# Kernel tuning notes

Measured on AMD Instinct MI355X. Metric: run time of the kernel, lower is better.

Reference implementation:

```python
import jax, jax.numpy as jnp
import numpy as np

N, D_IN, D_H, D_ATT, C_CLUST, N_CLS = 10000, 1024, 512, 256, 10, 4


def setup_inputs() -> dict:
    key = jax.random.key(0)
    ks = jax.random.split(key, 20)
    s = 0.02
    return {
        "x": jax.random.normal(ks[0], (N, D_IN), dtype=jnp.float32),
        "cluster_id": jax.random.randint(ks[1], (N,), 0, C_CLUST, dtype=jnp.int64),
        # per-cluster phi: Linear(1024->512) + ReLU + Linear(512->512) + ReLU
        "W1": s * jax.random.normal(ks[2], (C_CLUST, D_IN, D_H), dtype=jnp.float32),
        "b1": jnp.zeros((C_CLUST, D_H), dtype=jnp.float32),
        "W2": s * jax.random.normal(ks[3], (C_CLUST, D_H, D_H), dtype=jnp.float32),
        "b2": jnp.zeros((C_CLUST, D_H), dtype=jnp.float32),
        # attention_net fc: Linear(512->512)+ReLU
        "Wfc": s * jax.random.normal(ks[4], (D_H, D_H), dtype=jnp.float32),
        "bfc": jnp.zeros((D_H,), dtype=jnp.float32),
        # Attn_Net_Gated
        "Wa": s * jax.random.normal(ks[5], (D_H, D_ATT), dtype=jnp.float32),
        "ba": jnp.zeros((D_ATT,), dtype=jnp.float32),
        "Wb": s * jax.random.normal(ks[6], (D_H, D_ATT), dtype=jnp.float32),
        "bb": jnp.zeros((D_ATT,), dtype=jnp.float32),
        "Wc": s * jax.random.normal(ks[7], (D_ATT, 1), dtype=jnp.float32),
        "bc": jnp.zeros((1,), dtype=jnp.float32),
        # rho: Linear(512->256)+ReLU
        "Wr": s * jax.random.normal(ks[8], (D_H, D_ATT), dtype=jnp.float32),
        "br": jnp.zeros((D_ATT,), dtype=jnp.float32),
        # classifier: Linear(256->4)
        "Wcls": s * jax.random.normal(ks[9], (D_ATT, N_CLS), dtype=jnp.float32),
        "bcls": jnp.zeros((N_CLS,), dtype=jnp.float32),
    }


def reference(x, cluster_id, W1, b1, W2, b2, Wfc, bfc, Wa, ba, Wb, bb, Wc, bc, Wr, br, Wcls, bcls):
    C = W1.shape[0]
    # dense dispatch: apply every cluster's phi, then masked-mean per cluster
    # (ReLU is per-point elementwise, so masked mean == mean over members)
    h1 = jax.nn.relu(jnp.einsum('nd,cdh->cnh', x, W1) + b1[:, None, :])   # [C,N,512]
    h2 = jax.nn.relu(jnp.einsum('cnh,chk->cnk', h1, W2) + b2[:, None, :]) # [C,N,512]
    mask = (cluster_id[None, :] == jnp.arange(C)[:, None]).astype(h2.dtype)  # [C,N]
    counts = jnp.maximum(mask.sum(axis=1), 1.0)                           # [C]
    pooled = jnp.einsum('cnk,cn->ck', h2, mask) / counts[:, None]         # [C,512]
    # attention_net: fc + gated attention
    h = jax.nn.relu(pooled @ Wfc + bfc)                                   # [C,512]
    gate = jnp.tanh(h @ Wa + ba) * jax.nn.sigmoid(h @ Wb + bb)            # [C,256]
    A = (gate @ Wc + bc)                                                  # [C,1]
    A = jax.nn.softmax(A.T, axis=1)                                       # [1,C]
    h_path = A @ h                                                        # [1,512]
    hr = jax.nn.relu(h_path @ Wr + br)                                    # [1,256]
    logits = (hr[0] @ Wcls + bcls)[None, :]                               # [1,4]
    Y_prob = jax.nn.softmax(logits, axis=1)
    Y_hat = jnp.argmax(logits, axis=1)[:, None]
    return logits, Y_prob, Y_hat
```

## Files before the change

kernel.cpp:

```cpp
#include <hip/hip_runtime.h>
#include <math.h>

#define DIN 1024
#define DH 512
#define DATT 256
#define CNUM 10
#define NCLS 4

typedef __attribute__((ext_vector_type(8))) short bf16x8;
typedef __attribute__((ext_vector_type(4))) float f32x4;
typedef unsigned short ushort_t;
typedef unsigned int uint_t;

__device__ inline ushort_t f2bf(float f) {
    uint_t u = __float_as_uint(f);
    u += 0x7FFF + ((u >> 16) & 1);
    return (ushort_t)(u >> 16);
}

__device__ inline void gl_lds16(const void* g, void* l) {
    __builtin_amdgcn_global_load_lds(
        (const __attribute__((address_space(1))) unsigned int*)g,
        (__attribute__((address_space(3))) unsigned int*)l, 16, 0, 0);
}


__global__ __launch_bounds__(1024) void k_bucket(
    const int* __restrict__ cid, int n, const float* __restrict__ bc,
    int* __restrict__ counts_g, int* __restrict__ offsets_g, int* __restrict__ tile_off_g,
    int* __restrict__ bucket, float* __restrict__ pooled, float* __restrict__ a_logit)
{
    __shared__ int h[CNUM], off[CNUM + 1], cur[CNUM], toff[CNUM + 1];
    int t = threadIdx.x;
    int lane = t & 63;
    if (t < CNUM) { h[t] = 0; cur[t] = 0; }
    __syncthreads();

    for (int i = t; i < n; i += 1024) {
        int c = cid[i];
        #pragma unroll
        for (int cc = 0; cc < CNUM; cc++) {
            unsigned long long mask = __ballot(c == cc);
            if (mask == 0ull) continue;
            int leader = __ffsll(mask) - 1;
            if (lane == leader) atomicAdd(&h[cc], __popcll(mask));
        }
    }
    __syncthreads();
    if (t == 0) {
        int a = 0, tt = 0;
        for (int c = 0; c < CNUM; c++) {
            off[c] = a; toff[c] = tt;
            a += h[c]; tt += (h[c] + 127) >> 7;
        }
        off[CNUM] = a; toff[CNUM] = tt;
    }
    __syncthreads();
    if (t < CNUM) counts_g[t] = h[t];
    if (t <= CNUM) { offsets_g[t] = off[t]; tile_off_g[t] = toff[t]; }
    if (t < CNUM) a_logit[t] = bc[0];

    for (int i = t; i < n; i += 1024) {
        int c = cid[i];
        #pragma unroll
        for (int cc = 0; cc < CNUM; cc++) {
            unsigned long long mask = __ballot(c == cc);
            if (mask == 0ull) continue;
            int leader = __ffsll(mask) - 1;
            int basep = 0;
            if (lane == leader) basep = atomicAdd(&cur[cc], __popcll(mask));
            basep = __shfl(basep, leader, 64);
            if (c == cc) {
                int rank = __popcll(mask & ((1ull << lane) - 1ull));
                bucket[off[cc] + basep + rank] = i;
            }
        }
    }
    for (int i = t; i < CNUM * DH; i += 1024) pooled[i] = 0.f;
}


__global__ __launch_bounds__(256) void k_castx(
    const float* __restrict__ x, const int* __restrict__ bucket,
    ushort_t* __restrict__ xb, int n)
{
    int row = blockIdx.x * 2 + (threadIdx.x >> 7);
    if (row >= n) return;
    int col = (threadIdx.x & 127) * 8;
    const float* src = x + (size_t)bucket[row] * DIN + col;
    float4 v0 = *(const float4*)(src);
    float4 v1 = *(const float4*)(src + 4);
    ushort4 o0 = make_ushort4(f2bf(v0.x), f2bf(v0.y), f2bf(v0.z), f2bf(v0.w));
    ushort4 o1 = make_ushort4(f2bf(v1.x), f2bf(v1.y), f2bf(v1.z), f2bf(v1.w));
    ushort_t* dst = xb + (size_t)row * DIN + col;
    *(ushort4*)dst = o0;
    *(ushort4*)(dst + 4) = o1;
}

__global__ __launch_bounds__(256) void k_castw(
    const float* __restrict__ W1, const float* __restrict__ W2,
    ushort_t* __restrict__ W1t, ushort_t* __restrict__ W2t)
{
    __shared__ float tile[64][65];
    int z = blockIdx.z;
    const float* src; ushort_t* dst; int K;
    if (z < CNUM) { K = DIN; src = W1 + (size_t)z * K * DH; dst = W1t + (size_t)z * DH * K; }
    else          { K = DH;  src = W2 + (size_t)(z - CNUM) * K * DH; dst = W2t + (size_t)(z - CNUM) * DH * K; }
    int k0 = blockIdx.x * 64;
    if (k0 >= K) return;
    int n0 = blockIdx.y * 64;
    int t = threadIdx.x;
    int rr = t >> 4;
    int cc = (t & 15) * 4;
    #pragma unroll
    for (int i = 0; i < 4; i++) {
        int row = rr + 16 * i;
        float4 v = *(const float4*)(src + (size_t)(k0 + row) * DH + n0 + cc);
        tile[row][cc + 0] = v.x; tile[row][cc + 1] = v.y;
        tile[row][cc + 2] = v.z; tile[row][cc + 3] = v.w;
    }
    __syncthreads();
    #pragma unroll
    for (int i = 0; i < 4; i++) {
        int nrow = rr + 16 * i;
        ushort4 o = make_ushort4(f2bf(tile[cc + 0][nrow]), f2bf(tile[cc + 1][nrow]),
                                 f2bf(tile[cc + 2][nrow]), f2bf(tile[cc + 3][nrow]));
        *(ushort4*)(dst + (size_t)(n0 + nrow) * K + k0 + cc) = o;
    }
}


__device__ inline void gemm_tile(
    const ushort_t* __restrict__ A, const ushort_t* __restrict__ Wt,
    int Kd, int base, int cnt, int m0, int tile_n, int c,
    f32x4 acc[4][4], ushort_t As[128][32], ushort_t Bs[128][32])
{
    int t = threadIdx.x;
    int lane = t & 63;
    int w = t >> 6, wr = w >> 1, wc = w & 1;
    int m = lane & 15, quad = lane >> 4;

    int r0 = t >> 2;
    int kc = (t & 3) * 8;

    int ra0 = m0 + r0;      if (ra0 > cnt - 1) ra0 = cnt - 1;
    int ra1 = m0 + 64 + r0; if (ra1 > cnt - 1) ra1 = cnt - 1;
    const ushort_t* aSrc0 = A + (size_t)(base + ra0) * Kd + kc;
    const ushort_t* aSrc1 = A + (size_t)(base + ra1) * Kd + kc;
    const ushort_t* bSrc0 = Wt + ((size_t)c * DH + tile_n + r0) * Kd + kc;
    const ushort_t* bSrc1 = Wt + ((size_t)c * DH + tile_n + 64 + r0) * Kd + kc;

    ushort_t* aDst0 = &As[r0][kc];
    ushort_t* aDst1 = &As[64 + r0][kc];
    ushort_t* bDst0 = &Bs[r0][kc];
    ushort_t* bDst1 = &Bs[64 + r0][kc];

    const ushort_t* aF = &As[64 * wr + m][quad * 8];
    const ushort_t* bF = &Bs[64 * wc + m][quad * 8];

    for (int k0 = 0; k0 < Kd; k0 += 32) {
        __syncthreads();
        gl_lds16(aSrc0 + k0, aDst0);
        gl_lds16(aSrc1 + k0, aDst1);
        gl_lds16(bSrc0 + k0, bDst0);
        gl_lds16(bSrc1 + k0, bDst1);
        __syncthreads();
        bf16x8 a[4], b[4];
        #pragma unroll
        for (int mf = 0; mf < 4; mf++) a[mf] = *(const bf16x8*)(aF + mf * 16 * 32);
        #pragma unroll
        for (int nf = 0; nf < 4; nf++) b[nf] = *(const bf16x8*)(bF + nf * 16 * 32);
        #pragma unroll
        for (int mf = 0; mf < 4; mf++)
            #pragma unroll
            for (int nf = 0; nf < 4; nf++)
                acc[mf][nf] = __builtin_amdgcn_mfma_f32_16x16x32_bf16(a[mf], b[nf], acc[mf][nf], 0, 0, 0);
    }
}

__global__ __launch_bounds__(256, 1) void k_mfma1(
    const ushort_t* __restrict__ xb, const ushort_t* __restrict__ W1t,
    const float* __restrict__ b1,
    const int* __restrict__ offsets, const int* __restrict__ counts,
    const int* __restrict__ tile_off,
    ushort_t* __restrict__ H1)
{
    __shared__ ushort_t As[128][32];
    __shared__ ushort_t Bs[128][32];
    int tx = blockIdx.x;
    if (tx >= tile_off[CNUM]) return;
    int c = 0;
    while (tx >= tile_off[c + 1]) c++;
    int m0 = (tx - tile_off[c]) * 128;
    int base = offsets[c], cnt = counts[c];
    int tile_n = blockIdx.y * 128;

    f32x4 acc[4][4] = {};
    gemm_tile(xb, W1t, DIN, base, cnt, m0, tile_n, c, acc, As, Bs);

    int t = threadIdx.x, lane = t & 63;
    int w = t >> 6, wr = w >> 1, wc = w & 1;
    int m = lane & 15, quad = lane >> 4;
    int col0 = tile_n + 64 * wc;
    #pragma unroll
    for (int nf = 0; nf < 4; nf++) {
        int col = col0 + 16 * nf + m;
        float bv = b1[c * DH + col];
        #pragma unroll
        for (int mf = 0; mf < 4; mf++) {
            int rowb = m0 + 64 * wr + 16 * mf + quad * 4;
            #pragma unroll
            for (int r = 0; r < 4; r++) {
                int row = rowb + r;
                if (row < cnt)
                    H1[(size_t)(base + row) * DH + col] = f2bf(fmaxf(acc[mf][nf][r] + bv, 0.f));
            }
        }
    }
}

__global__ __launch_bounds__(256, 1) void k_mfma2(
    const ushort_t* __restrict__ H1, const ushort_t* __restrict__ W2t,
    const float* __restrict__ b2,
    const int* __restrict__ offsets, const int* __restrict__ counts,
    const int* __restrict__ tile_off,
    float* __restrict__ pooled)
{
    __shared__ ushort_t As[128][32];
    __shared__ ushort_t Bs[128][32];
    int tx = blockIdx.x;
    if (tx >= tile_off[CNUM]) return;
    int c = 0;
    while (tx >= tile_off[c + 1]) c++;
    int m0 = (tx - tile_off[c]) * 128;
    int base = offsets[c], cnt = counts[c];
    int tile_n = blockIdx.y * 128;

    f32x4 acc[4][4] = {};
    gemm_tile(H1, W2t, DH, base, cnt, m0, tile_n, c, acc, As, Bs);

    int t = threadIdx.x, lane = t & 63;
    int w = t >> 6, wr = w >> 1, wc = w & 1;
    int m = lane & 15, quad = lane >> 4;
    int col0 = tile_n + 64 * wc;
    #pragma unroll
    for (int nf = 0; nf < 4; nf++) {
        int col = col0 + 16 * nf + m;
        float bv = b2[c * DH + col];
        float s = 0.f;
        #pragma unroll
        for (int mf = 0; mf < 4; mf++) {
            int rowb = m0 + 64 * wr + 16 * mf + quad * 4;
            #pragma unroll
            for (int r = 0; r < 4; r++) {
                int row = rowb + r;
                if (row < cnt) s += fmaxf(acc[mf][nf][r] + bv, 0.f);
            }
        }
        s += __shfl_xor(s, 16);
        s += __shfl_xor(s, 32);
        if (quad == 0) atomicAdd(&pooled[c * DH + col], s);
    }
}


#define MT 64
#define NT 128
#define KT 32

__global__ __launch_bounds__(256) void k_gemm1(
    const float* __restrict__ x, const float* __restrict__ W1, const float* __restrict__ b1,
    const int* __restrict__ bucket, const int* __restrict__ offsets, const int* __restrict__ counts,
    float* __restrict__ H1)
{
    int c = blockIdx.z;
    int cnt = counts[c];
    int m0 = blockIdx.x * MT;
    if (m0 >= cnt) return;
    int rows = min(MT, cnt - m0);
    int n0 = blockIdx.y * NT;
    int base = offsets[c];

    __shared__ float As[KT][MT + 4];
    __shared__ float Bs[KT][NT];

    int t = threadIdx.x;
    int tr = t >> 4;
    int tc = t & 15;
    int lr = t >> 2;
    int lk = (t & 3) * 8;
    const float* xrow = nullptr;
    if (lr < rows) xrow = x + (size_t)bucket[base + m0 + lr] * DIN;

    float acc[4][8];
    #pragma unroll
    for (int i = 0; i < 4; i++)
        #pragma unroll
        for (int j = 0; j < 8; j++) acc[i][j] = 0.f;

    const float* Wp = W1 + (size_t)c * DIN * DH + n0;

    for (int k0 = 0; k0 < DIN; k0 += KT) {
        __syncthreads();
        if (xrow) {
            float4 v0 = *(const float4*)(xrow + k0 + lk);
            float4 v1 = *(const float4*)(xrow + k0 + lk + 4);
            As[lk + 0][lr] = v0.x; As[lk + 1][lr] = v0.y;
            As[lk + 2][lr] = v0.z; As[lk + 3][lr] = v0.w;
            As[lk + 4][lr] = v1.x; As[lk + 5][lr] = v1.y;
            As[lk + 6][lr] = v1.z; As[lk + 7][lr] = v1.w;
        } else {
            #pragma unroll
            for (int i = 0; i < 8; i++) As[lk + i][lr] = 0.f;
        }
        #pragma unroll
        for (int i = 0; i < 4; i++) {
            int idx = i * 256 + t;
            int kk = idx >> 5;
            int cv = idx & 31;
            *(float4*)&Bs[kk][cv * 4] = *(const float4*)(Wp + (size_t)(k0 + kk) * DH + cv * 4);
        }
        __syncthreads();
        #pragma unroll
        for (int k = 0; k < KT; k++) {
            float4 av  = *(const float4*)&As[k][4 * tr];
            float4 bv0 = *(const float4*)&Bs[k][4 * tc];
            float4 bv1 = *(const float4*)&Bs[k][64 + 4 * tc];
            float a[4] = {av.x, av.y, av.z, av.w};
            float b[8] = {bv0.x, bv0.y, bv0.z, bv0.w, bv1.x, bv1.y, bv1.z, bv1.w};
            #pragma unroll
            for (int i = 0; i < 4; i++)
                #pragma unroll
                for (int j = 0; j < 8; j++)
                    acc[i][j] = fmaf(a[i], b[j], acc[i][j]);
        }
    }

    #pragma unroll
    for (int i = 0; i < 4; i++) {
        int r = 4 * tr + i;
        if (r < rows) {
            size_t grow = (size_t)(base + m0 + r) * DH;
            #pragma unroll
            for (int j = 0; j < 8; j++) {
                int cidx = (j < 4) ? (4 * tc + j) : (64 + 4 * tc + (j - 4));
                int col = n0 + cidx;
                float v = acc[i][j] + b1[c * DH + col];
                H1[grow + col] = fmaxf(v, 0.f);
            }
        }
    }
}

__global__ __launch_bounds__(256) void k_gemm2(
    const float* __restrict__ H1, const float* __restrict__ W2, const float* __restrict__ b2,
    const int* __restrict__ offsets, const int* __restrict__ counts,
    float* __restrict__ pooled)
{
    int c = blockIdx.z;
    int cnt = counts[c];
    int m0 = blockIdx.x * MT;
    if (m0 >= cnt) return;
    int rows = min(MT, cnt - m0);
    int n0 = blockIdx.y * NT;
    int base = offsets[c];

    __shared__ float As[KT][MT + 4];
    __shared__ float Bs[KT][NT];
    __shared__ float red[16][NT];

    int t = threadIdx.x;
    int tr = t >> 4;
    int tc = t & 15;
    int lr = t >> 2;
    int lk = (t & 3) * 8;
    const float* arow = (lr < rows) ? (H1 + (size_t)(base + m0 + lr) * DH) : nullptr;

    float acc[4][8];
    #pragma unroll
    for (int i = 0; i < 4; i++)
        #pragma unroll
        for (int j = 0; j < 8; j++) acc[i][j] = 0.f;

    const float* Wp = W2 + (size_t)c * DH * DH + n0;

    for (int k0 = 0; k0 < DH; k0 += KT) {
        __syncthreads();
        if (arow) {
            float4 v0 = *(const float4*)(arow + k0 + lk);
            float4 v1 = *(const float4*)(arow + k0 + lk + 4);
            As[lk + 0][lr] = v0.x; As[lk + 1][lr] = v0.y;
            As[lk + 2][lr] = v0.z; As[lk + 3][lr] = v0.w;
            As[lk + 4][lr] = v1.x; As[lk + 5][lr] = v1.y;
            As[lk + 6][lr] = v1.z; As[lk + 7][lr] = v1.w;
        } else {
            #pragma unroll
            for (int i = 0; i < 8; i++) As[lk + i][lr] = 0.f;
        }
        #pragma unroll
        for (int i = 0; i < 4; i++) {
            int idx = i * 256 + t;
            int kk = idx >> 5;
            int cv = idx & 31;
            *(float4*)&Bs[kk][cv * 4] = *(const float4*)(Wp + (size_t)(k0 + kk) * DH + cv * 4);
        }
        __syncthreads();
        #pragma unroll
        for (int k = 0; k < KT; k++) {
            float4 av  = *(const float4*)&As[k][4 * tr];
            float4 bv0 = *(const float4*)&Bs[k][4 * tc];
            float4 bv1 = *(const float4*)&Bs[k][64 + 4 * tc];
            float a[4] = {av.x, av.y, av.z, av.w};
            float b[8] = {bv0.x, bv0.y, bv0.z, bv0.w, bv1.x, bv1.y, bv1.z, bv1.w};
            #pragma unroll
            for (int i = 0; i < 4; i++)
                #pragma unroll
                for (int j = 0; j < 8; j++)
                    acc[i][j] = fmaf(a[i], b[j], acc[i][j]);
        }
    }

    __syncthreads();
    #pragma unroll
    for (int j = 0; j < 8; j++) {
        int cidx = (j < 4) ? (4 * tc + j) : (64 + 4 * tc + (j - 4));
        float bias = b2[c * DH + n0 + cidx];
        float s = 0.f;
        #pragma unroll
        for (int i = 0; i < 4; i++) {
            if (4 * tr + i < rows) s += fmaxf(acc[i][j] + bias, 0.f);
        }
        red[tr][cidx] = s;
    }
    __syncthreads();
    if (t < NT) {
        float s = 0.f;
        #pragma unroll
        for (int r = 0; r < 16; r++) s += red[r][t];
        atomicAdd(&pooled[c * DH + n0 + t], s);
    }
}


__global__ __launch_bounds__(256) void k_fc2(
    const float* __restrict__ pooled, const int* __restrict__ counts,
    const float* __restrict__ Wfc, const float* __restrict__ bfc,
    float* __restrict__ hfc)
{
    int c = blockIdx.x;
    int c0 = blockIdx.y * 64;
    __shared__ float ps[DH];
    __shared__ float red[4][64];
    int t = threadIdx.x;
    float cnt = fmaxf((float)counts[c], 1.f);
    ps[t] = pooled[c * DH + t] / cnt;
    ps[t + 256] = pooled[c * DH + t + 256] / cnt;
    __syncthreads();
    int col = c0 + (t & 63);
    int ks = t >> 6;
    float acc = 0.f;
    #pragma unroll 8
    for (int k = ks * 128; k < ks * 128 + 128; k++)
        acc = fmaf(ps[k], Wfc[(size_t)k * DH + col], acc);
    red[ks][t & 63] = acc;
    __syncthreads();
    if (t < 64) {
        float v = red[0][t] + red[1][t] + red[2][t] + red[3][t] + bfc[c0 + t];
        hfc[c * DH + c0 + t] = fmaxf(v, 0.f);
    }
}

__global__ __launch_bounds__(256) void k_gate2(
    const float* __restrict__ hfc,
    const float* __restrict__ Wa, const float* __restrict__ ba,
    const float* __restrict__ Wb, const float* __restrict__ bb,
    const float* __restrict__ Wc,
    float* __restrict__ a_logit)
{
    int c = blockIdx.x;
    int d0 = blockIdx.y * 64;
    __shared__ float hf[DH];
    __shared__ float ra[4][64], rb[4][64];
    int t = threadIdx.x;
    hf[t] = hfc[c * DH + t];
    hf[t + 256] = hfc[c * DH + t + 256];
    __syncthreads();
    int d = d0 + (t & 63);
    int ks = t >> 6;
    float ga = 0.f, gb = 0.f;
    #pragma unroll 8
    for (int k = ks * 128; k < ks * 128 + 128; k++) {
        float h = hf[k];
        ga = fmaf(h, Wa[(size_t)k * DATT + d], ga);
        gb = fmaf(h, Wb[(size_t)k * DATT + d], gb);
    }
    ra[ks][t & 63] = ga;
    rb[ks][t & 63] = gb;
    __syncthreads();
    if (t < 64) {
        float sa = ra[0][t] + ra[1][t] + ra[2][t] + ra[3][t] + ba[d0 + t];
        float sb = rb[0][t] + rb[1][t] + rb[2][t] + rb[3][t] + bb[d0 + t];
        float g = tanhf(sa) * (1.f / (1.f + expf(-sb)));
        float p = g * Wc[d0 + t];
        #pragma unroll
        for (int off = 32; off >= 1; off >>= 1) p += __shfl_down(p, off, 64);
        if (t == 0) atomicAdd(&a_logit[c], p);
    }
}

__global__ __launch_bounds__(1024) void k_final(
    const float* __restrict__ hfc, const float* __restrict__ a_logit,
    const float* __restrict__ Wr, const float* __restrict__ br,
    const float* __restrict__ Wcls, const float* __restrict__ bcls,
    float* __restrict__ out)
{
    int t = threadIdx.x;
    __shared__ float hp[DH];
    __shared__ float r1[4][DATT];
    __shared__ float hr[DATT];
    __shared__ float wred[4][NCLS];

    float al[CNUM];
    float m = -1e30f;
    #pragma unroll
    for (int c = 0; c < CNUM; c++) { al[c] = a_logit[c]; m = fmaxf(m, al[c]); }
    float s = 0.f;
    #pragma unroll
    for (int c = 0; c < CNUM; c++) { al[c] = expf(al[c] - m); s += al[c]; }
    float inv = 1.f / s;

    if (t < DH) {
        float v = 0.f;
        #pragma unroll
        for (int c = 0; c < CNUM; c++) v = fmaf(al[c] * inv, hfc[c * DH + t], v);
        hp[t] = v;
    }
    __syncthreads();

    int d = t & 255;
    int ks = t >> 8;
    float acc = 0.f;
    #pragma unroll 8
    for (int k = ks * 128; k < ks * 128 + 128; k++)
        acc = fmaf(hp[k], Wr[(size_t)k * DATT + d], acc);
    r1[ks][d] = acc;
    __syncthreads();
    if (t < DATT)
        hr[t] = fmaxf(r1[0][t] + r1[1][t] + r1[2][t] + r1[3][t] + br[t], 0.f);
    __syncthreads();

    if (t < 256) {
        float h = hr[t];
        #pragma unroll
        for (int cls = 0; cls < NCLS; cls++) {
            float p = h * Wcls[(size_t)t * NCLS + cls];
            #pragma unroll
            for (int off = 32; off >= 1; off >>= 1) p += __shfl_down(p, off, 64);
            if ((t & 63) == 0) wred[t >> 6][cls] = p;
        }
    }
    __syncthreads();
    if (t == 0) {
        float lg[NCLS];
        #pragma unroll
        for (int cls = 0; cls < NCLS; cls++)
            lg[cls] = bcls[cls] + wred[0][cls] + wred[1][cls] + wred[2][cls] + wred[3][cls];
        float mm = lg[0];
        #pragma unroll
        for (int i = 1; i < NCLS; i++) mm = fmaxf(mm, lg[i]);
        float ss = 0.f, pr[NCLS];
        #pragma unroll
        for (int i = 0; i < NCLS; i++) { pr[i] = expf(lg[i] - mm); ss += pr[i]; }
        int am = 0; float best = lg[0];
        #pragma unroll
        for (int i = 1; i < NCLS; i++) if (lg[i] > best) { best = lg[i]; am = i; }
        #pragma unroll
        for (int i = 0; i < NCLS; i++) out[i] = lg[i];
        #pragma unroll
        for (int i = 0; i < NCLS; i++) out[4 + i] = pr[i] / ss;
        out[8] = (float)am;
    }
}


extern "C" void kernel_launch(void* const* d_in, const int* in_sizes, int n_in,
                              void* d_out, int out_size, void* d_ws, size_t ws_size,
                              hipStream_t stream) {
    (void)n_in; (void)out_size;
    const float* x    = (const float*)d_in[0];
    const int*   cid  = (const int*)d_in[1];
    const float* W1   = (const float*)d_in[2];
    const float* b1   = (const float*)d_in[3];
    const float* W2   = (const float*)d_in[4];
    const float* b2   = (const float*)d_in[5];
    const float* Wfc  = (const float*)d_in[6];
    const float* bfc  = (const float*)d_in[7];
    const float* Wa   = (const float*)d_in[8];
    const float* ba   = (const float*)d_in[9];
    const float* Wb   = (const float*)d_in[10];
    const float* bb   = (const float*)d_in[11];
    const float* Wc   = (const float*)d_in[12];
    const float* bc   = (const float*)d_in[13];
    const float* Wr   = (const float*)d_in[14];
    const float* br   = (const float*)d_in[15];
    const float* Wcls = (const float*)d_in[16];
    const float* bcls = (const float*)d_in[17];
    float* out = (float*)d_out;
    float* ws  = (float*)d_ws;

    int n = in_sizes[1];

    float* pooled   = ws + 0;
    int*   counts   = (int*)(ws + 5120);
    int*   offsets  = (int*)(ws + 5136);
    int*   tile_off = (int*)(ws + 5152);
    float* a_logit  = ws + 5168;
    float* hfc      = ws + 5184;
    int*   bucket   = (int*)(ws + 10304);

    size_t big0 = (((size_t)(10304 + n) * 4) + 255) & ~(size_t)255;
    size_t w1t_bytes = (size_t)CNUM * DH * DIN * 2;
    size_t w2t_bytes = (size_t)CNUM * DH * DH * 2;
    size_t h1_bytes  = (size_t)n * DH * 2;
    size_t xb_bytes  = (size_t)n * DIN * 2;
    size_t need = big0 + w1t_bytes + w2t_bytes + h1_bytes + xb_bytes;

    k_bucket<<<1, 1024, 0, stream>>>(cid, n, bc, counts, offsets, tile_off, bucket, pooled, a_logit);

    if (ws_size >= need) {
        ushort_t* W1t = (ushort_t*)((char*)d_ws + big0);
        ushort_t* W2t = (ushort_t*)((char*)d_ws + big0 + w1t_bytes);
        ushort_t* H1  = (ushort_t*)((char*)d_ws + big0 + w1t_bytes + w2t_bytes);
        ushort_t* xb  = (ushort_t*)((char*)d_ws + big0 + w1t_bytes + w2t_bytes + h1_bytes);

        k_castx<<<(n + 1) / 2, 256, 0, stream>>>(x, bucket, xb, n);
        k_castw<<<dim3(DIN / 64, DH / 64, 2 * CNUM), 256, 0, stream>>>(W1, W2, W1t, W2t);

        int maxt = n / 128 + CNUM;
        k_mfma1<<<dim3(maxt, DH / 128), 256, 0, stream>>>(xb, W1t, b1, offsets, counts, tile_off, H1);
        k_mfma2<<<dim3(maxt, DH / 128), 256, 0, stream>>>(H1, W2t, b2, offsets, counts, tile_off, pooled);
    } else {
        float* H1f = ws + ((10304 + n + 31) & ~31);
        dim3 gg((n + MT - 1) / MT, DH / NT, CNUM);
        k_gemm1<<<gg, 256, 0, stream>>>(x, W1, b1, bucket, offsets, counts, H1f);
        k_gemm2<<<gg, 256, 0, stream>>>(H1f, W2, b2, offsets, counts, pooled);
    }

    k_fc2<<<dim3(CNUM, 8), 256, 0, stream>>>(pooled, counts, Wfc, bfc, hfc);
    k_gate2<<<dim3(CNUM, 4), 256, 0, stream>>>(hfc, Wa, ba, Wb, bb, Wc, a_logit);
    k_final<<<1, 1024, 0, stream>>>(hfc, a_logit, Wr, br, Wcls, bcls, out);
}
```

Before: 259.7 us.

## Fuse x cast, both phi GEMMs and pooling into one kernel

```diff
diff --git a/kernel.cpp b/kernel.cpp
--- a/kernel.cpp
+++ b/kernel.cpp
@@ -6,6 +6,7 @@
 #define DATT 256
 #define CNUM 10
 #define NCLS 4
+#define ROWS 32
 
 typedef __attribute__((ext_vector_type(8))) short bf16x8;
 typedef __attribute__((ext_vector_type(4))) float f32x4;
@@ -51,7 +52,7 @@
         int a = 0, tt = 0;
         for (int c = 0; c < CNUM; c++) {
             off[c] = a; toff[c] = tt;
-            a += h[c]; tt += (h[c] + 127) >> 7;
+            a += h[c]; tt += (h[c] + ROWS - 1) / ROWS;
         }
         off[CNUM] = a; toff[CNUM] = tt;
     }
@@ -80,23 +81,6 @@
 }
 
 
-__global__ __launch_bounds__(256) void k_castx(
-    const float* __restrict__ x, const int* __restrict__ bucket,
-    ushort_t* __restrict__ xb, int n)
-{
-    int row = blockIdx.x * 2 + (threadIdx.x >> 7);
-    if (row >= n) return;
-    int col = (threadIdx.x & 127) * 8;
-    const float* src = x + (size_t)bucket[row] * DIN + col;
-    float4 v0 = *(const float4*)(src);
-    float4 v1 = *(const float4*)(src + 4);
-    ushort4 o0 = make_ushort4(f2bf(v0.x), f2bf(v0.y), f2bf(v0.z), f2bf(v0.w));
-    ushort4 o1 = make_ushort4(f2bf(v1.x), f2bf(v1.y), f2bf(v1.z), f2bf(v1.w));
-    ushort_t* dst = xb + (size_t)row * DIN + col;
-    *(ushort4*)dst = o0;
-    *(ushort4*)(dst + 4) = o1;
-}
-
 __global__ __launch_bounds__(256) void k_castw(
     const float* __restrict__ W1, const float* __restrict__ W2,
     ushort_t* __restrict__ W1t, ushort_t* __restrict__ W2t)
@@ -130,136 +114,136 @@
 }
 
 
-__device__ inline void gemm_tile(
-    const ushort_t* __restrict__ A, const ushort_t* __restrict__ Wt,
-    int Kd, int base, int cnt, int m0, int tile_n, int c,
-    f32x4 acc[4][4], ushort_t As[128][32], ushort_t Bs[128][32])
-{
-    int t = threadIdx.x;
-    int lane = t & 63;
-    int w = t >> 6, wr = w >> 1, wc = w & 1;
-    int m = lane & 15, quad = lane >> 4;
-
-    int r0 = t >> 2;
-    int kc = (t & 3) * 8;
-
-    int ra0 = m0 + r0;      if (ra0 > cnt - 1) ra0 = cnt - 1;
-    int ra1 = m0 + 64 + r0; if (ra1 > cnt - 1) ra1 = cnt - 1;
-    const ushort_t* aSrc0 = A + (size_t)(base + ra0) * Kd + kc;
-    const ushort_t* aSrc1 = A + (size_t)(base + ra1) * Kd + kc;
-    const ushort_t* bSrc0 = Wt + ((size_t)c * DH + tile_n + r0) * Kd + kc;
-    const ushort_t* bSrc1 = Wt + ((size_t)c * DH + tile_n + 64 + r0) * Kd + kc;
-
-    ushort_t* aDst0 = &As[r0][kc];
-    ushort_t* aDst1 = &As[64 + r0][kc];
-    ushort_t* bDst0 = &Bs[r0][kc];
-    ushort_t* bDst1 = &Bs[64 + r0][kc];
-
-    const ushort_t* aF = &As[64 * wr + m][quad * 8];
-    const ushort_t* bF = &Bs[64 * wc + m][quad * 8];
-
-    for (int k0 = 0; k0 < Kd; k0 += 32) {
-        __syncthreads();
-        gl_lds16(aSrc0 + k0, aDst0);
-        gl_lds16(aSrc1 + k0, aDst1);
-        gl_lds16(bSrc0 + k0, bDst0);
-        gl_lds16(bSrc1 + k0, bDst1);
-        __syncthreads();
-        bf16x8 a[4], b[4];
-        #pragma unroll
-        for (int mf = 0; mf < 4; mf++) a[mf] = *(const bf16x8*)(aF + mf * 16 * 32);
-        #pragma unroll
-        for (int nf = 0; nf < 4; nf++) b[nf] = *(const bf16x8*)(bF + nf * 16 * 32);
-        #pragma unroll
-        for (int mf = 0; mf < 4; mf++)
-            #pragma unroll
-            for (int nf = 0; nf < 4; nf++)
-                acc[mf][nf] = __builtin_amdgcn_mfma_f32_16x16x32_bf16(a[mf], b[nf], acc[mf][nf], 0, 0, 0);
-    }
-}
-
-__global__ __launch_bounds__(256, 1) void k_mfma1(
-    const ushort_t* __restrict__ xb, const ushort_t* __restrict__ W1t,
-    const float* __restrict__ b1,
+__global__ __launch_bounds__(256, 1) void k_phi(
+    const float* __restrict__ x, const int* __restrict__ bucket,
+    const ushort_t* __restrict__ W1t, const ushort_t* __restrict__ W2t,
+    const float* __restrict__ b1, const float* __restrict__ b2,
     const int* __restrict__ offsets, const int* __restrict__ counts,
     const int* __restrict__ tile_off,
-    ushort_t* __restrict__ H1)
-{
-    __shared__ ushort_t As[128][32];
-    __shared__ ushort_t Bs[128][32];
+    float* __restrict__ pooled)
+{
+    __shared__ ushort_t As[ROWS][32];
+    __shared__ ushort_t Bs[256][32];
+    __shared__ ushort_t H1s[16][ROWS][32];
+
     int tx = blockIdx.x;
     if (tx >= tile_off[CNUM]) return;
     int c = 0;
     while (tx >= tile_off[c + 1]) c++;
-    int m0 = (tx - tile_off[c]) * 128;
+    int m0 = (tx - tile_off[c]) * ROWS;
     int base = offsets[c], cnt = counts[c];
-    int tile_n = blockIdx.y * 128;
-
-    f32x4 acc[4][4] = {};
-    gemm_tile(xb, W1t, DIN, base, cnt, m0, tile_n, c, acc, As, Bs);
 
     int t = threadIdx.x, lane = t & 63;
-    int w = t >> 6, wr = w >> 1, wc = w & 1;
+    int w = t >> 6;
     int m = lane & 15, quad = lane >> 4;
-    int col0 = tile_n + 64 * wc;
-    #pragma unroll
-    for (int nf = 0; nf < 4; nf++) {
-        int col = col0 + 16 * nf + m;
-        float bv = b1[c * DH + col];
-        #pragma unroll
-        for (int mf = 0; mf < 4; mf++) {
-            int rowb = m0 + 64 * wr + 16 * mf + quad * 4;
-            #pragma unroll
-            for (int r = 0; r < 4; r++) {
-                int row = rowb + r;
-                if (row < cnt)
-                    H1[(size_t)(base + row) * DH + col] = f2bf(fmaxf(acc[mf][nf][r] + bv, 0.f));
+
+    int ar = t >> 3;
+    int akc = (t & 7) * 4;
+    int arow = m0 + ar; if (arow > cnt - 1) arow = cnt - 1;
+    const float* aPtr = x + (size_t)bucket[base + arow] * DIN + akc;
+
+    char* bsDst = (char*)&Bs[0][0] + 16 * t;
+    int bRow = t >> 2;
+    int bKc = (t & 3) * 8;
+
+    const ushort_t* aF0 = &As[m][quad * 8];
+    const ushort_t* aF1 = &As[16 + m][quad * 8];
+    const ushort_t* bF  = &Bs[64 * w + m][quad * 8];
+
+    f32x4 acc[2][4];
+
+    #pragma unroll
+    for (int p = 0; p < 2; p++) {
+        #pragma unroll
+        for (int mf = 0; mf < 2; mf++)
+            #pragma unroll
+            for (int nf = 0; nf < 4; nf++) acc[mf][nf] = (f32x4)(0.f);
+
+        const ushort_t* wp = W1t + ((size_t)c * DH + p * 256 + bRow) * DIN + bKc;
+
+        for (int k0 = 0; k0 < DIN; k0 += 32) {
+            __syncthreads();
+            float4 av = *(const float4*)(aPtr + k0);
+            *(ushort4*)&As[ar][akc] =
+                make_ushort4(f2bf(av.x), f2bf(av.y), f2bf(av.z), f2bf(av.w));
+            #pragma unroll
+            for (int i = 0; i < 4; i++)
+                gl_lds16(wp + k0 + (size_t)(64 * i) * DIN, bsDst + 4096 * i);
+            __syncthreads();
+
+            bf16x8 a0 = *(const bf16x8*)aF0;
+            bf16x8 a1 = *(const bf16x8*)aF1;
+            bf16x8 b[4];
+            #pragma unroll
+            for (int nf = 0; nf < 4; nf++) b[nf] = *(const bf16x8*)(bF + nf * 512);
+            #pragma unroll
+            for (int nf = 0; nf < 4; nf++) {
+                acc[0][nf] = __builtin_amdgcn_mfma_f32_16x16x32_bf16(a0, b[nf], acc[0][nf], 0, 0, 0);
+                acc[1][nf] = __builtin_amdgcn_mfma_f32_16x16x32_bf16(a1, b[nf], acc[1][nf], 0, 0, 0);
             }
         }
-    }
-}
-
-__global__ __launch_bounds__(256, 1) void k_mfma2(
-    const ushort_t* __restrict__ H1, const ushort_t* __restrict__ W2t,
-    const float* __restrict__ b2,
-    const int* __restrict__ offsets, const int* __restrict__ counts,
-    const int* __restrict__ tile_off,
-    float* __restrict__ pooled)
-{
-    __shared__ ushort_t As[128][32];
-    __shared__ ushort_t Bs[128][32];
-    int tx = blockIdx.x;
-    if (tx >= tile_off[CNUM]) return;
-    int c = 0;
-    while (tx >= tile_off[c + 1]) c++;
-    int m0 = (tx - tile_off[c]) * 128;
-    int base = offsets[c], cnt = counts[c];
-    int tile_n = blockIdx.y * 128;
-
-    f32x4 acc[4][4] = {};
-    gemm_tile(H1, W2t, DH, base, cnt, m0, tile_n, c, acc, As, Bs);
-
-    int t = threadIdx.x, lane = t & 63;
-    int w = t >> 6, wr = w >> 1, wc = w & 1;
-    int m = lane & 15, quad = lane >> 4;
-    int col0 = tile_n + 64 * wc;
-    #pragma unroll
-    for (int nf = 0; nf < 4; nf++) {
-        int col = col0 + 16 * nf + m;
-        float bv = b2[c * DH + col];
-        float s = 0.f;
-        #pragma unroll
-        for (int mf = 0; mf < 4; mf++) {
-            int rowb = m0 + 64 * wr + 16 * mf + quad * 4;
-            #pragma unroll
-            for (int r = 0; r < 4; r++) {
-                int row = rowb + r;
-                if (row < cnt) s += fmaxf(acc[mf][nf][r] + bv, 0.f);
+
+        #pragma unroll
+        for (int nf = 0; nf < 4; nf++) {
+            int colL = 64 * w + 16 * nf + m;
+            int col = p * 256 + colL;
+            float bv = b1[c * DH + col];
+            int chunk = p * 8 + (colL >> 5);
+            int ck = colL & 31;
+            #pragma unroll
+            for (int mf = 0; mf < 2; mf++)
+                #pragma unroll
+                for (int r = 0; r < 4; r++)
+                    H1s[chunk][16 * mf + quad * 4 + r][ck] =
+                        f2bf(fmaxf(acc[mf][nf][r] + bv, 0.f));
+        }
+    }
+
+    #pragma unroll
+    for (int p = 0; p < 2; p++) {
+        #pragma unroll
+        for (int mf = 0; mf < 2; mf++)
+            #pragma unroll
+            for (int nf = 0; nf < 4; nf++) acc[mf][nf] = (f32x4)(0.f);
+
+        const ushort_t* wp = W2t + ((size_t)c * DH + p * 256 + bRow) * DH + bKc;
+
+        for (int k0 = 0; k0 < DH; k0 += 32) {
+            __syncthreads();
+            #pragma unroll
+            for (int i = 0; i < 4; i++)
+                gl_lds16(wp + k0 + (size_t)(64 * i) * DH, bsDst + 4096 * i);
+            __syncthreads();
+
+            const ushort_t* h = &H1s[k0 >> 5][0][0];
+            bf16x8 a0 = *(const bf16x8*)(h + m * 32 + quad * 8);
+            bf16x8 a1 = *(const bf16x8*)(h + (16 + m) * 32 + quad * 8);
+            bf16x8 b[4];
+            #pragma unroll
+            for (int nf = 0; nf < 4; nf++) b[nf] = *(const bf16x8*)(bF + nf * 512);
+            #pragma unroll
+            for (int nf = 0; nf < 4; nf++) {
+                acc[0][nf] = __builtin_amdgcn_mfma_f32_16x16x32_bf16(a0, b[nf], acc[0][nf], 0, 0, 0);
+                acc[1][nf] = __builtin_amdgcn_mfma_f32_16x16x32_bf16(a1, b[nf], acc[1][nf], 0, 0, 0);
             }
         }
-        s += __shfl_xor(s, 16);
-        s += __shfl_xor(s, 32);
-        if (quad == 0) atomicAdd(&pooled[c * DH + col], s);
+
+        #pragma unroll
+        for (int nf = 0; nf < 4; nf++) {
+            int col = p * 256 + 64 * w + 16 * nf + m;
+            float bv = b2[c * DH + col];
+            float s = 0.f;
+            #pragma unroll
+            for (int mf = 0; mf < 2; mf++)
+                #pragma unroll
+                for (int r = 0; r < 4; r++) {
+                    int row = m0 + 16 * mf + quad * 4 + r;
+                    if (row < cnt) s += fmaxf(acc[mf][nf][r] + bv, 0.f);
+                }
+            s += __shfl_xor(s, 16);
+            s += __shfl_xor(s, 32);
+            if (quad == 0) atomicAdd(&pooled[c * DH + col], s);
+        }
     }
 }
 
@@ -621,24 +605,19 @@
     size_t big0 = (((size_t)(10304 + n) * 4) + 255) & ~(size_t)255;
     size_t w1t_bytes = (size_t)CNUM * DH * DIN * 2;
     size_t w2t_bytes = (size_t)CNUM * DH * DH * 2;
-    size_t h1_bytes  = (size_t)n * DH * 2;
-    size_t xb_bytes  = (size_t)n * DIN * 2;
-    size_t need = big0 + w1t_bytes + w2t_bytes + h1_bytes + xb_bytes;
+    size_t need = big0 + w1t_bytes + w2t_bytes;
 
     k_bucket<<<1, 1024, 0, stream>>>(cid, n, bc, counts, offsets, tile_off, bucket, pooled, a_logit);
 
     if (ws_size >= need) {
         ushort_t* W1t = (ushort_t*)((char*)d_ws + big0);
         ushort_t* W2t = (ushort_t*)((char*)d_ws + big0 + w1t_bytes);
-        ushort_t* H1  = (ushort_t*)((char*)d_ws + big0 + w1t_bytes + w2t_bytes);
-        ushort_t* xb  = (ushort_t*)((char*)d_ws + big0 + w1t_bytes + w2t_bytes + h1_bytes);
-
-        k_castx<<<(n + 1) / 2, 256, 0, stream>>>(x, bucket, xb, n);
+
         k_castw<<<dim3(DIN / 64, DH / 64, 2 * CNUM), 256, 0, stream>>>(W1, W2, W1t, W2t);
 
-        int maxt = n / 128 + CNUM;
-        k_mfma1<<<dim3(maxt, DH / 128), 256, 0, stream>>>(xb, W1t, b1, offsets, counts, tile_off, H1);
-        k_mfma2<<<dim3(maxt, DH / 128), 256, 0, stream>>>(H1, W2t, b2, offsets, counts, tile_off, pooled);
+        int maxt = (n + ROWS - 1) / ROWS + CNUM;
+        k_phi<<<maxt, 256, 0, stream>>>(x, bucket, W1t, W2t, b1, b2,
+                                        offsets, counts, tile_off, pooled);
     } else {
         float* H1f = ws + ((10304 + n + 31) & ~31);
         dim3 gg((n + MT - 1) / MT, DH / NT, CNUM);
```

After: 277.0 us. +6.7%, slower.

## Fuse bucketing and bf16 casts into one prep kernel, gather rows in GEMM1

Applied to the files above, without the earlier changes.

```diff
diff --git a/kernel.cpp b/kernel.cpp
--- a/kernel.cpp
+++ b/kernel.cpp
@@ -25,91 +25,97 @@
 }
 
 
-__global__ __launch_bounds__(1024) void k_bucket(
-    const int* __restrict__ cid, int n, const float* __restrict__ bc,
+__global__ __launch_bounds__(256) void k_prep(
+    const float* __restrict__ x, const int* __restrict__ cid, int n,
+    const float* __restrict__ bc,
+    const float* __restrict__ W1, const float* __restrict__ W2,
+    ushort_t* __restrict__ xb, ushort_t* __restrict__ W1t, ushort_t* __restrict__ W2t,
+    int do_cast,
     int* __restrict__ counts_g, int* __restrict__ offsets_g, int* __restrict__ tile_off_g,
     int* __restrict__ bucket, float* __restrict__ pooled, float* __restrict__ a_logit)
 {
-    __shared__ int h[CNUM], off[CNUM + 1], cur[CNUM], toff[CNUM + 1];
-    int t = threadIdx.x;
-    int lane = t & 63;
-    if (t < CNUM) { h[t] = 0; cur[t] = 0; }
-    __syncthreads();
-
-    for (int i = t; i < n; i += 1024) {
-        int c = cid[i];
-        #pragma unroll
-        for (int cc = 0; cc < CNUM; cc++) {
-            unsigned long long mask = __ballot(c == cc);
-            if (mask == 0ull) continue;
-            int leader = __ffsll(mask) - 1;
-            if (lane == leader) atomicAdd(&h[cc], __popcll(mask));
-        }
-    }
-    __syncthreads();
-    if (t == 0) {
-        int a = 0, tt = 0;
-        for (int c = 0; c < CNUM; c++) {
-            off[c] = a; toff[c] = tt;
-            a += h[c]; tt += (h[c] + 127) >> 7;
-        }
-        off[CNUM] = a; toff[CNUM] = tt;
-    }
-    __syncthreads();
-    if (t < CNUM) counts_g[t] = h[t];
-    if (t <= CNUM) { offsets_g[t] = off[t]; tile_off_g[t] = toff[t]; }
-    if (t < CNUM) a_logit[t] = bc[0];
-
-    for (int i = t; i < n; i += 1024) {
-        int c = cid[i];
-        #pragma unroll
-        for (int cc = 0; cc < CNUM; cc++) {
-            unsigned long long mask = __ballot(c == cc);
-            if (mask == 0ull) continue;
-            int leader = __ffsll(mask) - 1;
-            int basep = 0;
-            if (lane == leader) basep = atomicAdd(&cur[cc], __popcll(mask));
-            basep = __shfl(basep, leader, 64);
-            if (c == cc) {
-                int rank = __popcll(mask & ((1ull << lane) - 1ull));
-                bucket[off[cc] + basep + rank] = i;
+    int bid = blockIdx.x;
+    int t = threadIdx.x;
+
+    if (bid == 0) {
+        __shared__ int h[CNUM], off[CNUM + 1], cur[CNUM], toff[CNUM + 1];
+        int lane = t & 63;
+        if (t < CNUM) { h[t] = 0; cur[t] = 0; }
+        __syncthreads();
+
+        for (int i = t; i < n; i += 256) {
+            int c = cid[i];
+            #pragma unroll
+            for (int cc = 0; cc < CNUM; cc++) {
+                unsigned long long mask = __ballot(c == cc);
+                if (mask == 0ull) continue;
+                int leader = __ffsll(mask) - 1;
+                if (lane == leader) atomicAdd(&h[cc], __popcll(mask));
             }
         }
-    }
-    for (int i = t; i < CNUM * DH; i += 1024) pooled[i] = 0.f;
-}
-
-
-__global__ __launch_bounds__(256) void k_castx(
-    const float* __restrict__ x, const int* __restrict__ bucket,
-    ushort_t* __restrict__ xb, int n)
-{
-    int row = blockIdx.x * 2 + (threadIdx.x >> 7);
-    if (row >= n) return;
-    int col = (threadIdx.x & 127) * 8;
-    const float* src = x + (size_t)bucket[row] * DIN + col;
-    float4 v0 = *(const float4*)(src);
-    float4 v1 = *(const float4*)(src + 4);
-    ushort4 o0 = make_ushort4(f2bf(v0.x), f2bf(v0.y), f2bf(v0.z), f2bf(v0.w));
-    ushort4 o1 = make_ushort4(f2bf(v1.x), f2bf(v1.y), f2bf(v1.z), f2bf(v1.w));
-    ushort_t* dst = xb + (size_t)row * DIN + col;
-    *(ushort4*)dst = o0;
-    *(ushort4*)(dst + 4) = o1;
-}
-
-__global__ __launch_bounds__(256) void k_castw(
-    const float* __restrict__ W1, const float* __restrict__ W2,
-    ushort_t* __restrict__ W1t, ushort_t* __restrict__ W2t)
-{
+        __syncthreads();
+        if (t == 0) {
+            int a = 0, tt = 0;
+            for (int c = 0; c < CNUM; c++) {
+                off[c] = a; toff[c] = tt;
+                a += h[c]; tt += (h[c] + 127) >> 7;
+            }
+            off[CNUM] = a; toff[CNUM] = tt;
+        }
+        __syncthreads();
+        if (t < CNUM) counts_g[t] = h[t];
+        if (t <= CNUM) { offsets_g[t] = off[t]; tile_off_g[t] = toff[t]; }
+        if (t < CNUM) a_logit[t] = bc[0];
+
+        for (int i = t; i < n; i += 256) {
+            int c = cid[i];
+            #pragma unroll
+            for (int cc = 0; cc < CNUM; cc++) {
+                unsigned long long mask = __ballot(c == cc);
+                if (mask == 0ull) continue;
+                int leader = __ffsll(mask) - 1;
+                int basep = 0;
+                if (lane == leader) basep = atomicAdd(&cur[cc], __popcll(mask));
+                basep = __shfl(basep, leader, 64);
+                if (c == cc) {
+                    int rank = __popcll(mask & ((1ull << lane) - 1ull));
+                    bucket[off[cc] + basep + rank] = i;
+                }
+            }
+        }
+        for (int i = t; i < CNUM * DH; i += 256) pooled[i] = 0.f;
+        return;
+    }
+
+    if (!do_cast) return;
+
+    int nxb = (n + 1) / 2;
+    int idx = bid - 1;
+    if (idx < nxb) {
+        int row = idx * 2 + (t >> 7);
+        if (row >= n) return;
+        int col = (t & 127) * 8;
+        const float* src = x + (size_t)row * DIN + col;
+        float4 v0 = *(const float4*)(src);
+        float4 v1 = *(const float4*)(src + 4);
+        ushort_t* dst = xb + (size_t)row * DIN + col;
+        *(ushort4*)dst = make_ushort4(f2bf(v0.x), f2bf(v0.y), f2bf(v0.z), f2bf(v0.w));
+        *(ushort4*)(dst + 4) = make_ushort4(f2bf(v1.x), f2bf(v1.y), f2bf(v1.z), f2bf(v1.w));
+        return;
+    }
+
     __shared__ float tile[64][65];
-    int z = blockIdx.z;
+    int widx = idx - nxb;
+    int z = widx >> 7;
+    if (z >= 2 * CNUM) return;
+    int kx = (widx & 127) >> 3;
+    int ny = widx & 7;
     const float* src; ushort_t* dst; int K;
     if (z < CNUM) { K = DIN; src = W1 + (size_t)z * K * DH; dst = W1t + (size_t)z * DH * K; }
     else          { K = DH;  src = W2 + (size_t)(z - CNUM) * K * DH; dst = W2t + (size_t)(z - CNUM) * DH * K; }
-    int k0 = blockIdx.x * 64;
+    int k0 = kx * 64;
     if (k0 >= K) return;
-    int n0 = blockIdx.y * 64;
-    int t = threadIdx.x;
+    int n0 = ny * 64;
     int rr = t >> 4;
     int cc = (t & 15) * 4;
     #pragma unroll
@@ -131,8 +137,8 @@
 
 
 __device__ inline void gemm_tile(
-    const ushort_t* __restrict__ A, const ushort_t* __restrict__ Wt,
-    int Kd, int base, int cnt, int m0, int tile_n, int c,
+    const ushort_t* aSrc0, const ushort_t* aSrc1,
+    const ushort_t* bSrc0, const ushort_t* bSrc1, int Kd,
     f32x4 acc[4][4], ushort_t As[128][32], ushort_t Bs[128][32])
 {
     int t = threadIdx.x;
@@ -142,13 +148,6 @@
 
     int r0 = t >> 2;
     int kc = (t & 3) * 8;
-
-    int ra0 = m0 + r0;      if (ra0 > cnt - 1) ra0 = cnt - 1;
-    int ra1 = m0 + 64 + r0; if (ra1 > cnt - 1) ra1 = cnt - 1;
-    const ushort_t* aSrc0 = A + (size_t)(base + ra0) * Kd + kc;
-    const ushort_t* aSrc1 = A + (size_t)(base + ra1) * Kd + kc;
-    const ushort_t* bSrc0 = Wt + ((size_t)c * DH + tile_n + r0) * Kd + kc;
-    const ushort_t* bSrc1 = Wt + ((size_t)c * DH + tile_n + 64 + r0) * Kd + kc;
 
     ushort_t* aDst0 = &As[r0][kc];
     ushort_t* aDst1 = &As[64 + r0][kc];
@@ -180,7 +179,7 @@
 
 __global__ __launch_bounds__(256, 1) void k_mfma1(
     const ushort_t* __restrict__ xb, const ushort_t* __restrict__ W1t,
-    const float* __restrict__ b1,
+    const float* __restrict__ b1, const int* __restrict__ bucket,
     const int* __restrict__ offsets, const int* __restrict__ counts,
     const int* __restrict__ tile_off,
     ushort_t* __restrict__ H1)
@@ -195,10 +194,20 @@
     int base = offsets[c], cnt = counts[c];
     int tile_n = blockIdx.y * 128;
 
+    int t = threadIdx.x;
+    int r0 = t >> 2;
+    int kc = (t & 3) * 8;
+    int ra0 = m0 + r0;      if (ra0 > cnt - 1) ra0 = cnt - 1; if (ra0 < 0) ra0 = 0;
+    int ra1 = m0 + 64 + r0; if (ra1 > cnt - 1) ra1 = cnt - 1; if (ra1 < 0) ra1 = 0;
+    const ushort_t* aSrc0 = xb + (size_t)bucket[base + ra0] * DIN + kc;
+    const ushort_t* aSrc1 = xb + (size_t)bucket[base + ra1] * DIN + kc;
+    const ushort_t* bSrc0 = W1t + ((size_t)c * DH + tile_n + r0) * DIN + kc;
+    const ushort_t* bSrc1 = W1t + ((size_t)c * DH + tile_n + 64 + r0) * DIN + kc;
+
     f32x4 acc[4][4] = {};
-    gemm_tile(xb, W1t, DIN, base, cnt, m0, tile_n, c, acc, As, Bs);
-
-    int t = threadIdx.x, lane = t & 63;
+    gemm_tile(aSrc0, aSrc1, bSrc0, bSrc1, DIN, acc, As, Bs);
+
+    int lane = t & 63;
     int w = t >> 6, wr = w >> 1, wc = w & 1;
     int m = lane & 15, quad = lane >> 4;
     int col0 = tile_n + 64 * wc;
@@ -236,10 +245,20 @@
     int base = offsets[c], cnt = counts[c];
     int tile_n = blockIdx.y * 128;
 
+    int t = threadIdx.x;
+    int r0 = t >> 2;
+    int kc = (t & 3) * 8;
+    int ra0 = m0 + r0;      if (ra0 > cnt - 1) ra0 = cnt - 1; if (ra0 < 0) ra0 = 0;
+    int ra1 = m0 + 64 + r0; if (ra1 > cnt - 1) ra1 = cnt - 1; if (ra1 < 0) ra1 = 0;
+    const ushort_t* aSrc0 = H1 + (size_t)(base + ra0) * DH + kc;
+    const ushort_t* aSrc1 = H1 + (size_t)(base + ra1) * DH + kc;
+    const ushort_t* bSrc0 = W2t + ((size_t)c * DH + tile_n + r0) * DH + kc;
+    const ushort_t* bSrc1 = W2t + ((size_t)c * DH + tile_n + 64 + r0) * DH + kc;
+
     f32x4 acc[4][4] = {};
-    gemm_tile(H1, W2t, DH, base, cnt, m0, tile_n, c, acc, As, Bs);
-
-    int t = threadIdx.x, lane = t & 63;
+    gemm_tile(aSrc0, aSrc1, bSrc0, bSrc1, DH, acc, As, Bs);
+
+    int lane = t & 63;
     int w = t >> 6, wr = w >> 1, wc = w & 1;
     int m = lane & 15, quad = lane >> 4;
     int col0 = tile_n + 64 * wc;
@@ -625,19 +644,22 @@
     size_t xb_bytes  = (size_t)n * DIN * 2;
     size_t need = big0 + w1t_bytes + w2t_bytes + h1_bytes + xb_bytes;
 
-    k_bucket<<<1, 1024, 0, stream>>>(cid, n, bc, counts, offsets, tile_off, bucket, pooled, a_logit);
-
-    if (ws_size >= need) {
-        ushort_t* W1t = (ushort_t*)((char*)d_ws + big0);
-        ushort_t* W2t = (ushort_t*)((char*)d_ws + big0 + w1t_bytes);
-        ushort_t* H1  = (ushort_t*)((char*)d_ws + big0 + w1t_bytes + w2t_bytes);
-        ushort_t* xb  = (ushort_t*)((char*)d_ws + big0 + w1t_bytes + w2t_bytes + h1_bytes);
-
-        k_castx<<<(n + 1) / 2, 256, 0, stream>>>(x, bucket, xb, n);
-        k_castw<<<dim3(DIN / 64, DH / 64, 2 * CNUM), 256, 0, stream>>>(W1, W2, W1t, W2t);
-
+    ushort_t* W1t = (ushort_t*)((char*)d_ws + big0);
+    ushort_t* W2t = (ushort_t*)((char*)d_ws + big0 + w1t_bytes);
+    ushort_t* H1  = (ushort_t*)((char*)d_ws + big0 + w1t_bytes + w2t_bytes);
+    ushort_t* xb  = (ushort_t*)((char*)d_ws + big0 + w1t_bytes + w2t_bytes + h1_bytes);
+
+    int fast = (ws_size >= need) ? 1 : 0;
+    int nxb = (n + 1) / 2;
+    int prep_blocks = fast ? (1 + nxb + 128 * 2 * CNUM) : 1;
+
+    k_prep<<<prep_blocks, 256, 0, stream>>>(
+        x, cid, n, bc, W1, W2, xb, W1t, W2t, fast,
+        counts, offsets, tile_off, bucket, pooled, a_logit);
+
+    if (fast) {
         int maxt = n / 128 + CNUM;
-        k_mfma1<<<dim3(maxt, DH / 128), 256, 0, stream>>>(xb, W1t, b1, offsets, counts, tile_off, H1);
+        k_mfma1<<<dim3(maxt, DH / 128), 256, 0, stream>>>(xb, W1t, b1, bucket, offsets, counts, tile_off, H1);
         k_mfma2<<<dim3(maxt, DH / 128), 256, 0, stream>>>(H1, W2t, b2, offsets, counts, tile_off, pooled);
     } else {
         float* H1f = ws + ((10304 + n + 31) & ~31);
```

Result: slower. 320.5 us (+23.4%).
